# Performance work log

Measured on AMD Instinct MI355X. Metric: run time of the kernel, lower is better.

## Reference

```python
import jax, jax.numpy as jnp
import numpy as np

EPS = 1e-5

def setup_inputs() -> dict:
    key = jax.random.key(0)
    ks = jax.random.split(key, 8)
    N, C, ST, LT = 32, 2048, 16, 400
    ALPHA, K, BETA, CK = 4, 3, 4, 3
    Cb = C // BETA
    inp = {
        'st_feat': jax.random.normal(ks[0], (N, C, ST, 1, 1), dtype=jnp.float32),
        'lt_feat': jax.random.normal(ks[1], (N, C, LT, 1, 1), dtype=jnp.float32),
        # global branch G: Linear(ST->ST*alpha) -> BN1d -> ReLU -> Linear(->K) -> softmax
        'g_w1': jax.random.normal(ks[2], (ST * ALPHA, ST), dtype=jnp.float32) * 0.02,
        'g_bn_gamma': jnp.ones((ST * ALPHA,), jnp.float32),
        'g_bn_beta': jnp.zeros((ST * ALPHA,), jnp.float32),
        'g_bn_mean': jnp.zeros((ST * ALPHA,), jnp.float32),
        'g_bn_var': jnp.ones((ST * ALPHA,), jnp.float32),
        'g_w2': jax.random.normal(ks[3], (K, ST * ALPHA), dtype=jnp.float32) * 0.02,
        # local branch L: Conv1d(C->C/beta,k=3) -> BN1d -> ReLU -> Conv1d(C/beta->C,1) -> sigmoid
        'l_w1': jax.random.normal(ks[4], (Cb, C, CK), dtype=jnp.float32) * 0.02,
        'l_bn_gamma': jnp.ones((Cb,), jnp.float32),
        'l_bn_beta': jnp.zeros((Cb,), jnp.float32),
        'l_bn_mean': jnp.zeros((Cb,), jnp.float32),
        'l_bn_var': jnp.ones((Cb,), jnp.float32),
        'l_w2': jax.random.normal(ks[5], (C, Cb), dtype=jnp.float32) * 0.02,
    }
    return inp


def reference(st_feat, lt_feat, g_w1, g_bn_gamma, g_bn_beta, g_bn_mean, g_bn_var,
              g_w2, l_w1, l_bn_gamma, l_bn_beta, l_bn_mean, l_bn_var, l_w2):
    N, C, ST = st_feat.shape[:3]
    LT = lt_feat.shape[2]
    K = g_w2.shape[0]
    PAD = 1  # adaptive_convolution_padding; stride = 1
    # ---- global branch: per-(n,c) adaptive kernel (h=w=1 so avgpool is identity)
    st = st_feat.reshape(N * C, ST)                               # [NC, ST]
    h = st @ g_w1.T                                               # [NC, ST*alpha]
    h = (h - g_bn_mean) * jax.lax.rsqrt(g_bn_var + EPS) * g_bn_gamma + g_bn_beta
    h = jax.nn.relu(h)
    conv_kernel = jax.nn.softmax(h @ g_w2.T, axis=-1)             # [NC, K]
    # ---- local branch: channel-temporal sigmoid gate
    lt = lt_feat.reshape(N, C, LT)                                # [N, C, LT]
    x = jax.lax.conv_general_dilated(lt, l_w1, window_strides=(1,),
                                     padding=[(1, 1)],
                                     dimension_numbers=('NCH', 'OIH', 'NCH'))  # [N, C/beta, LT]
    x = (x - l_bn_mean[None, :, None]) * jax.lax.rsqrt(l_bn_var + EPS)[None, :, None] \
        * l_bn_gamma[None, :, None] + l_bn_beta[None, :, None]
    x = jax.nn.relu(x)
    gate = jax.nn.sigmoid(jnp.einsum('oc,nct->not', l_w2, x))     # [N, C, LT]
    new_lt = lt * gate
    # ---- temporal adaptive aggregation: per-(n,c) depthwise 1D conv, K taps
    kern = conv_kernel.reshape(N, C, K)
    xp = jnp.pad(new_lt, ((0, 0), (0, 0), (PAD, PAD)))            # [N, C, LT+2*PAD]
    out_len = LT + 2 * PAD - K + 1                                # == LT for K=3, PAD=1
    out = jnp.zeros((N, C, out_len), dtype=new_lt.dtype)
    for i in range(K):  # K is tiny (3)
        out = out + kern[:, :, i:i + 1] * xp[:, :, i:i + out_len]
    return out.reshape(N, C, out_len, 1, 1)
```

## Files before the change

kernel.cpp:

```cpp
#include <hip/hip_runtime.h>
#include <hip/hip_bf16.h>

#define N_   32
#define C_   2048
#define ST_  16
#define H_   64
#define K_   3
#define CB_  512
#define LT_  400
#define LTP_ 402

using bf16x8 = __attribute__((ext_vector_type(8))) __bf16;
using f32x4  = __attribute__((ext_vector_type(4))) float;
typedef unsigned short ushort_t;

__device__ __forceinline__ unsigned short f2bf(float f) {
    unsigned int u = __float_as_uint(f);
    u = (u + 0x7fffu + ((u >> 16) & 1u)) >> 16;
    return (unsigned short)u;
}
__device__ __forceinline__ float bf2f(unsigned short h) {
    return __uint_as_float(((unsigned int)h) << 16);
}

__global__ __launch_bounds__(256) void k_global(
    const float* __restrict__ st, const float* __restrict__ g_w1,
    const float* __restrict__ gam, const float* __restrict__ bet,
    const float* __restrict__ mean, const float* __restrict__ var,
    const float* __restrict__ g_w2, float* __restrict__ kern) {
    __shared__ float w1[H_][ST_];
    __shared__ float sc[H_], bi[H_];
    __shared__ float w2[K_][H_];
    int tid = threadIdx.x;
    for (int i = tid; i < H_ * ST_; i += 256) w1[i / ST_][i % ST_] = g_w1[i];
    if (tid < H_) {
        float s = gam[tid] * rsqrtf(var[tid] + 1e-5f);
        sc[tid] = s;
        bi[tid] = bet[tid] - mean[tid] * s;
    }
    for (int i = tid; i < K_ * H_; i += 256) w2[i / H_][i % H_] = g_w2[i];
    __syncthreads();
    int row = blockIdx.x * 256 + tid;
    const float* p = st + (size_t)row * ST_;
    float s[ST_];
#pragma unroll
    for (int i = 0; i < ST_; ++i) s[i] = p[i];
    float lg0 = 0.f, lg1 = 0.f, lg2 = 0.f;
    for (int j = 0; j < H_; ++j) {
        float h = 0.f;
#pragma unroll
        for (int i = 0; i < ST_; ++i) h = fmaf(w1[j][i], s[i], h);
        h = fmaxf(fmaf(h, sc[j], bi[j]), 0.f);
        lg0 = fmaf(w2[0][j], h, lg0);
        lg1 = fmaf(w2[1][j], h, lg1);
        lg2 = fmaf(w2[2][j], h, lg2);
    }
    float m = fmaxf(lg0, fmaxf(lg1, lg2));
    float e0 = __expf(lg0 - m), e1 = __expf(lg1 - m), e2 = __expf(lg2 - m);
    float inv = 1.f / (e0 + e1 + e2);
    float4 o = make_float4(e0 * inv, e1 * inv, e2 * inv, 0.f);
    *(float4*)(kern + (size_t)row * 4) = o;
}

__global__ __launch_bounds__(256) void k_transpose(
    const float* __restrict__ lt, ushort_t* __restrict__ ltT) {
    __shared__ float tile[32][33];
    int tt = blockIdx.x * 32;
    int cc = blockIdx.y * 32;
    int n  = blockIdx.z;
    const float* src = lt + ((size_t)n * C_ + cc) * LT_;
    int tx = threadIdx.x & 31, ty = threadIdx.x >> 5;
#pragma unroll
    for (int i = 0; i < 4; ++i) {
        int c = ty + i * 8;
        int t = tt + tx;
        tile[c][tx] = (t < LT_) ? src[(size_t)c * LT_ + t] : 0.f;
    }
    __syncthreads();
    ushort_t* dst = ltT + (size_t)n * LTP_ * C_;
#pragma unroll
    for (int i = 0; i < 4; ++i) {
        int tl = ty + i * 8;
        int t = tt + tl;
        if (t < LT_) dst[(size_t)(t + 1) * C_ + cc + tx] = f2bf(tile[tx][tl]);
    }
}

__global__ __launch_bounds__(256) void k_zero(ushort_t* __restrict__ ltT) {
    int i = blockIdx.x * 256 + threadIdx.x;
    int n = i >> 11, c = i & (C_ - 1);
    size_t base = (size_t)n * LTP_ * C_;
    ltT[base + c] = 0;
    ltT[base + (size_t)(LTP_ - 1) * C_ + c] = 0;
}

__global__ __launch_bounds__(256) void k_w1(
    const float* __restrict__ l_w1, ushort_t* __restrict__ w1b) {
    int i = blockIdx.x * 256 + threadIdx.x;
    float a = l_w1[(size_t)i * 3 + 0];
    float b = l_w1[(size_t)i * 3 + 1];
    float c = l_w1[(size_t)i * 3 + 2];
    w1b[0 * (size_t)CB_ * C_ + i] = f2bf(a);
    w1b[1 * (size_t)CB_ * C_ + i] = f2bf(b);
    w1b[2 * (size_t)CB_ * C_ + i] = f2bf(c);
}

__global__ __launch_bounds__(256) void k_w2(
    const float* __restrict__ l_w2, ushort_t* __restrict__ w2b) {
    int i = blockIdx.x * 256 + threadIdx.x;
    w2b[i] = f2bf(l_w2[i]);
}

#define BK  32
#define AST 40

__global__ __launch_bounds__(256, 2) void k_gemm1(
    const ushort_t* __restrict__ ltT, const ushort_t* __restrict__ w1b,
    const float* __restrict__ bn_g, const float* __restrict__ bn_b,
    const float* __restrict__ bn_m, const float* __restrict__ bn_v,
    ushort_t* __restrict__ Xws) {
    __shared__ __align__(16) ushort_t Asm[130 * AST];
    __shared__ __align__(16) ushort_t Bsm[384 * AST];
    const int tid = threadIdx.x;
    const int n   = blockIdx.z;
    const int tm  = blockIdx.x * 128;
    const int cb0 = blockIdx.y * 128;
    const int lane = tid & 63, lrow = lane & 15, quad = lane >> 4;
    const int wv = tid >> 6, wvM = wv & 1, wvN = wv >> 1;

    f32x4 acc[4][4];
#pragma unroll
    for (int i = 0; i < 4; ++i)
#pragma unroll
        for (int j = 0; j < 4; ++j) acc[i][j] = (f32x4){0.f, 0.f, 0.f, 0.f};

    const int r0 = tid >> 2, q = tid & 3;
    const ushort_t* aSrc0 = ltT + ((size_t)n * LTP_ + min(tm + r0, LTP_ - 1)) * C_ + q * 8;
    const ushort_t* aSrc1 = ltT + ((size_t)n * LTP_ + min(tm + r0 + 64, LTP_ - 1)) * C_ + q * 8;
    const ushort_t* aSrc2 = ltT + ((size_t)n * LTP_ + min(tm + r0 + 128, LTP_ - 1)) * C_ + q * 8;
    ushort_t* aDst0 = Asm + r0 * AST + q * 8;
    ushort_t* aDst1 = Asm + (r0 + 64) * AST + q * 8;
    ushort_t* aDst2 = Asm + (r0 + 128) * AST + q * 8;
    const ushort_t* bSrc = w1b + (size_t)(cb0 + r0) * C_ + q * 8;
    ushort_t* bDst = Bsm + r0 * AST + q * 8;
    constexpr int OFFB[6] = {0, 64, 512, 576, 1024, 1088};

    for (int c0 = 0; c0 < C_; c0 += BK) {
        __syncthreads();
        *(uint4*)aDst0 = *(const uint4*)aSrc0;
        *(uint4*)aDst1 = *(const uint4*)aSrc1;
        if (tid < 8) *(uint4*)aDst2 = *(const uint4*)aSrc2;
#pragma unroll
        for (int i = 0; i < 6; ++i)
            *(uint4*)(bDst + i * 64 * AST) = *(const uint4*)(bSrc + (size_t)OFFB[i] * C_);
        aSrc0 += BK; aSrc1 += BK; aSrc2 += BK; bSrc += BK;
        __syncthreads();

        bf16x8 bfr[3][4];
#pragma unroll
        for (int k = 0; k < 3; ++k)
#pragma unroll
            for (int nf = 0; nf < 4; ++nf)
                bfr[k][nf] = *(const bf16x8*)&Bsm[(k * 128 + wvN * 64 + nf * 16 + lrow) * AST + quad * 8];
#pragma unroll
        for (int mf = 0; mf < 4; ++mf) {
            bf16x8 af[3];
#pragma unroll
            for (int k = 0; k < 3; ++k)
                af[k] = *(const bf16x8*)&Asm[(wvM * 64 + mf * 16 + lrow + k) * AST + quad * 8];
#pragma unroll
            for (int nf = 0; nf < 4; ++nf)
#pragma unroll
                for (int k = 0; k < 3; ++k)
                    acc[mf][nf] = __builtin_amdgcn_mfma_f32_16x16x32_bf16(af[k], bfr[k][nf], acc[mf][nf], 0, 0, 0);
        }
    }
    float s[4], bo[4];
#pragma unroll
    for (int nf = 0; nf < 4; ++nf) {
        int cb = cb0 + wvN * 64 + nf * 16 + lrow;
        float sc = bn_g[cb] * rsqrtf(bn_v[cb] + 1e-5f);
        s[nf] = sc;
        bo[nf] = bn_b[cb] - bn_m[cb] * sc;
    }
    const int tBase = tm + wvM * 64 + quad * 4;
#pragma unroll
    for (int mf = 0; mf < 4; ++mf) {
#pragma unroll
        for (int r = 0; r < 4; ++r) {
            int t = tBase + mf * 16 + r;
            if (t < LT_) {
#pragma unroll
                for (int nf = 0; nf < 4; ++nf) {
                    int cb = cb0 + wvN * 64 + nf * 16 + lrow;
                    float v = fmaxf(fmaf(acc[mf][nf][r], s[nf], bo[nf]), 0.f);
                    Xws[((size_t)n * LT_ + t) * CB_ + cb] = f2bf(v);
                }
            }
        }
    }
}

__global__ __launch_bounds__(256, 2) void k_gemm2(
    const ushort_t* __restrict__ Xws, const ushort_t* __restrict__ w2b,
    ushort_t* __restrict__ gate) {
    __shared__ __align__(16) ushort_t Asm[128 * AST];
    __shared__ __align__(16) ushort_t Bsm[128 * AST];
    const int tid = threadIdx.x;
    const int n  = blockIdx.z;
    const int cm = blockIdx.x * 128;
    const int tt = blockIdx.y * 128;
    const int lane = tid & 63, lrow = lane & 15, quad = lane >> 4;
    const int wv = tid >> 6, wvM = wv & 1, wvN = wv >> 1;

    f32x4 acc[4][4];
#pragma unroll
    for (int i = 0; i < 4; ++i)
#pragma unroll
        for (int j = 0; j < 4; ++j) acc[i][j] = (f32x4){0.f, 0.f, 0.f, 0.f};

    const int r0 = tid >> 2, q = tid & 3;
    const ushort_t* aSrc0 = w2b + (size_t)(cm + r0) * CB_ + q * 8;
    const ushort_t* aSrc1 = w2b + (size_t)(cm + r0 + 64) * CB_ + q * 8;
    const ushort_t* bSrc0 = Xws + ((size_t)n * LT_ + min(tt + r0, LT_ - 1)) * CB_ + q * 8;
    const ushort_t* bSrc1 = Xws + ((size_t)n * LT_ + min(tt + r0 + 64, LT_ - 1)) * CB_ + q * 8;
    ushort_t* aDst0 = Asm + r0 * AST + q * 8;
    ushort_t* aDst1 = Asm + (r0 + 64) * AST + q * 8;
    ushort_t* bDst0 = Bsm + r0 * AST + q * 8;
    ushort_t* bDst1 = Bsm + (r0 + 64) * AST + q * 8;

    for (int k0 = 0; k0 < CB_; k0 += BK) {
        __syncthreads();
        *(uint4*)aDst0 = *(const uint4*)aSrc0;
        *(uint4*)aDst1 = *(const uint4*)aSrc1;
        *(uint4*)bDst0 = *(const uint4*)bSrc0;
        *(uint4*)bDst1 = *(const uint4*)bSrc1;
        aSrc0 += BK; aSrc1 += BK; bSrc0 += BK; bSrc1 += BK;
        __syncthreads();

        bf16x8 af[4], bfm[4];
#pragma unroll
        for (int mf = 0; mf < 4; ++mf)
            af[mf] = *(const bf16x8*)&Asm[(wvM * 64 + mf * 16 + lrow) * AST + quad * 8];
#pragma unroll
        for (int nf = 0; nf < 4; ++nf)
            bfm[nf] = *(const bf16x8*)&Bsm[(wvN * 64 + nf * 16 + lrow) * AST + quad * 8];
#pragma unroll
        for (int mf = 0; mf < 4; ++mf)
#pragma unroll
            for (int nf = 0; nf < 4; ++nf)
                acc[mf][nf] = __builtin_amdgcn_mfma_f32_16x16x32_bf16(af[mf], bfm[nf], acc[mf][nf], 0, 0, 0);
    }
#pragma unroll
    for (int mf = 0; mf < 4; ++mf) {
#pragma unroll
        for (int r = 0; r < 4; ++r) {
            int c = cm + wvM * 64 + mf * 16 + quad * 4 + r;
#pragma unroll
            for (int nf = 0; nf < 4; ++nf) {
                int t = tt + wvN * 64 + nf * 16 + lrow;
                if (t < LT_) {
                    float g = 1.f / (1.f + __expf(-acc[mf][nf][r]));
                    gate[((size_t)n * C_ + c) * LT_ + t] = f2bf(g);
                }
            }
        }
    }
}

__global__ __launch_bounds__(256) void k_final(
    const float* __restrict__ lt, const ushort_t* __restrict__ gate,
    const float* __restrict__ kern, float* __restrict__ out) {
    long long idx = (long long)blockIdx.x * 256 + threadIdx.x;
    int t0 = (int)(idx % 100) * 4;
    long long nc = idx / 100;
    const float*   ltp = lt   + (size_t)nc * LT_;
    const ushort_t* gp = gate + (size_t)nc * LT_;
    float4 kv = *(const float4*)(kern + (size_t)nc * 4);
    float nl[6];
#pragma unroll
    for (int j = -1; j <= 4; ++j) {
        int t = t0 + j;
        nl[j + 1] = (t >= 0 && t < LT_) ? ltp[t] * bf2f(gp[t]) : 0.f;
    }
    float4 o;
    o.x = kv.x * nl[0] + kv.y * nl[1] + kv.z * nl[2];
    o.y = kv.x * nl[1] + kv.y * nl[2] + kv.z * nl[3];
    o.z = kv.x * nl[2] + kv.y * nl[3] + kv.z * nl[4];
    o.w = kv.x * nl[3] + kv.y * nl[4] + kv.z * nl[5];
    *(float4*)(out + (size_t)nc * LT_ + t0) = o;
}

extern "C" void kernel_launch(void* const* d_in, const int* in_sizes, int n_in,
                              void* d_out, int out_size, void* d_ws, size_t ws_size,
                              hipStream_t stream) {
    const float* st   = (const float*)d_in[0];
    const float* lt   = (const float*)d_in[1];
    const float* g_w1 = (const float*)d_in[2];
    const float* g_bg = (const float*)d_in[3];
    const float* g_bb = (const float*)d_in[4];
    const float* g_bm = (const float*)d_in[5];
    const float* g_bv = (const float*)d_in[6];
    const float* g_w2 = (const float*)d_in[7];
    const float* l_w1 = (const float*)d_in[8];
    const float* l_bg = (const float*)d_in[9];
    const float* l_bb = (const float*)d_in[10];
    const float* l_bm = (const float*)d_in[11];
    const float* l_bv = (const float*)d_in[12];
    const float* l_w2 = (const float*)d_in[13];
    float* out = (float*)d_out;

    char* ws = (char*)d_ws;
    float*    kern = (float*)(ws + 0);
    ushort_t* w1b  = (ushort_t*)(ws + 1048576);
    ushort_t* w2b  = (ushort_t*)(ws + 7340032);
    ushort_t* Xws  = (ushort_t*)(ws + 9437184);
    ushort_t* ltT  = (ushort_t*)(ws + 22544384);
    ushort_t* gate = ltT;

    k_global<<<dim3((N_ * C_) / 256), dim3(256), 0, stream>>>(
        st, g_w1, g_bg, g_bb, g_bm, g_bv, g_w2, kern);
    k_w1<<<dim3((CB_ * C_) / 256), dim3(256), 0, stream>>>(l_w1, w1b);
    k_w2<<<dim3((C_ * CB_) / 256), dim3(256), 0, stream>>>(l_w2, w2b);
    k_zero<<<dim3((N_ * C_) / 256), dim3(256), 0, stream>>>(ltT);
    k_transpose<<<dim3(13, C_ / 32, N_), dim3(256), 0, stream>>>(lt, ltT);
    k_gemm1<<<dim3(4, 4, N_), dim3(256), 0, stream>>>(
        ltT, w1b, l_bg, l_bb, l_bm, l_bv, Xws);
    k_gemm2<<<dim3(C_ / 128, 4, N_), dim3(256), 0, stream>>>(Xws, w2b, gate);
    k_final<<<dim3((N_ * C_ * (LT_ / 4)) / 256), dim3(256), 0, stream>>>(
        lt, gate, kern, out);
}
```

Before: 445.6 us.

## Use direct global-to-LDS loads, flatten gemm2 over N*LT, fuse gating into gemm2

Both GEMMs now stage tiles into LDS with global_load_lds 16-byte loads into unpadded 32-element rows, replacing register round-trip copies. gemm1 is retiled to 64-wide output channel blocks with higher occupancy. gemm2 treats the batch and time dimensions as one flattened M dimension, which removes padding waste from the 400-row tiles. It also multiplies the gate by lt in its epilogue, so the final kernel reads one bf16 tensor instead of lt plus the gate. Unpadded LDS rows may cause bank conflicts, and the fused epilogue issues scattered fp32 reads of lt.

```diff
diff --git a/kernel.cpp b/kernel.cpp
--- a/kernel.cpp
+++ b/kernel.cpp
@@ -9,6 +9,7 @@
 #define CB_  512
 #define LT_  400
 #define LTP_ 402
+#define LTROWS_ (N_ * LTP_ + 144)
 
 using bf16x8 = __attribute__((ext_vector_type(8))) __bf16;
 using f32x4  = __attribute__((ext_vector_type(4))) float;
@@ -21,6 +22,12 @@
 }
 __device__ __forceinline__ float bf2f(unsigned short h) {
     return __uint_as_float(((unsigned int)h) << 16);
+}
+
+__device__ __forceinline__ void gload16(const ushort_t* g, ushort_t* l) {
+    __builtin_amdgcn_global_load_lds(
+        (const __attribute__((address_space(1))) unsigned int*)g,
+        (__attribute__((address_space(3))) unsigned int*)l, 16, 0, 0);
 }
 
 __global__ __launch_bounds__(256) void k_global(
@@ -111,74 +118,67 @@
     w2b[i] = f2bf(l_w2[i]);
 }
 
-#define BK  32
-#define AST 40
-
-__global__ __launch_bounds__(256, 2) void k_gemm1(
+#define BK 32
+
+__global__ __launch_bounds__(256, 4) void k_gemm1(
     const ushort_t* __restrict__ ltT, const ushort_t* __restrict__ w1b,
     const float* __restrict__ bn_g, const float* __restrict__ bn_b,
     const float* __restrict__ bn_m, const float* __restrict__ bn_v,
     ushort_t* __restrict__ Xws) {
-    __shared__ __align__(16) ushort_t Asm[130 * AST];
-    __shared__ __align__(16) ushort_t Bsm[384 * AST];
+    __shared__ __align__(16) ushort_t Asm[144 * 32];
+    __shared__ __align__(16) ushort_t Bsm[192 * 32];
     const int tid = threadIdx.x;
     const int n   = blockIdx.z;
     const int tm  = blockIdx.x * 128;
-    const int cb0 = blockIdx.y * 128;
+    const int cb0 = blockIdx.y * 64;
     const int lane = tid & 63, lrow = lane & 15, quad = lane >> 4;
     const int wv = tid >> 6, wvM = wv & 1, wvN = wv >> 1;
 
-    f32x4 acc[4][4];
+    f32x4 acc[4][2];
 #pragma unroll
     for (int i = 0; i < 4; ++i)
 #pragma unroll
-        for (int j = 0; j < 4; ++j) acc[i][j] = (f32x4){0.f, 0.f, 0.f, 0.f};
-
-    const int r0 = tid >> 2, q = tid & 3;
-    const ushort_t* aSrc0 = ltT + ((size_t)n * LTP_ + min(tm + r0, LTP_ - 1)) * C_ + q * 8;
-    const ushort_t* aSrc1 = ltT + ((size_t)n * LTP_ + min(tm + r0 + 64, LTP_ - 1)) * C_ + q * 8;
-    const ushort_t* aSrc2 = ltT + ((size_t)n * LTP_ + min(tm + r0 + 128, LTP_ - 1)) * C_ + q * 8;
-    ushort_t* aDst0 = Asm + r0 * AST + q * 8;
-    ushort_t* aDst1 = Asm + (r0 + 64) * AST + q * 8;
-    ushort_t* aDst2 = Asm + (r0 + 128) * AST + q * 8;
-    const ushort_t* bSrc = w1b + (size_t)(cb0 + r0) * C_ + q * 8;
-    ushort_t* bDst = Bsm + r0 * AST + q * 8;
-    constexpr int OFFB[6] = {0, 64, 512, 576, 1024, 1088};
+        for (int j = 0; j < 2; ++j) acc[i][j] = (f32x4){0.f, 0.f, 0.f, 0.f};
+
+    const ushort_t* aBase = ltT + ((size_t)n * LTP_ + tm + (lane >> 2)) * C_ + (lane & 3) * 8;
+    const ushort_t* bBase = w1b + ((size_t)cb0 + (lane >> 2)) * C_ + (lane & 3) * 8;
 
     for (int c0 = 0; c0 < C_; c0 += BK) {
         __syncthreads();
-        *(uint4*)aDst0 = *(const uint4*)aSrc0;
-        *(uint4*)aDst1 = *(const uint4*)aSrc1;
-        if (tid < 8) *(uint4*)aDst2 = *(const uint4*)aSrc2;
-#pragma unroll
-        for (int i = 0; i < 6; ++i)
-            *(uint4*)(bDst + i * 64 * AST) = *(const uint4*)(bSrc + (size_t)OFFB[i] * C_);
-        aSrc0 += BK; aSrc1 += BK; aSrc2 += BK; bSrc += BK;
+        for (int cc = wv; cc < 21; cc += 4) {
+            if (cc < 9) {
+                gload16(aBase + (size_t)cc * 16 * C_ + c0, Asm + cc * 512);
+            } else {
+                int j = cc - 9;
+                gload16(bBase + ((size_t)(j >> 2) * CB_ + (j & 3) * 16) * C_ + c0,
+                        Bsm + j * 512);
+            }
+        }
         __syncthreads();
 
-        bf16x8 bfr[3][4];
+        bf16x8 bfr[3][2];
 #pragma unroll
         for (int k = 0; k < 3; ++k)
 #pragma unroll
-            for (int nf = 0; nf < 4; ++nf)
-                bfr[k][nf] = *(const bf16x8*)&Bsm[(k * 128 + wvN * 64 + nf * 16 + lrow) * AST + quad * 8];
+            for (int nf = 0; nf < 2; ++nf)
+                bfr[k][nf] = *(const bf16x8*)&Bsm[(k * 64 + wvN * 32 + nf * 16 + lrow) * 32 + quad * 8];
 #pragma unroll
         for (int mf = 0; mf < 4; ++mf) {
             bf16x8 af[3];
 #pragma unroll
             for (int k = 0; k < 3; ++k)
-                af[k] = *(const bf16x8*)&Asm[(wvM * 64 + mf * 16 + lrow + k) * AST + quad * 8];
-#pragma unroll
-            for (int nf = 0; nf < 4; ++nf)
+                af[k] = *(const bf16x8*)&Asm[(wvM * 64 + mf * 16 + lrow + k) * 32 + quad * 8];
+#pragma unroll
+            for (int nf = 0; nf < 2; ++nf)
 #pragma unroll
                 for (int k = 0; k < 3; ++k)
                     acc[mf][nf] = __builtin_amdgcn_mfma_f32_16x16x32_bf16(af[k], bfr[k][nf], acc[mf][nf], 0, 0, 0);
         }
     }
-    float s[4], bo[4];
-#pragma unroll
-    for (int nf = 0; nf < 4; ++nf) {
-        int cb = cb0 + wvN * 64 + nf * 16 + lrow;
+    float s[2], bo[2];
+#pragma unroll
+    for (int nf = 0; nf < 2; ++nf) {
+        int cb = cb0 + wvN * 32 + nf * 16 + lrow;
         float sc = bn_g[cb] * rsqrtf(bn_v[cb] + 1e-5f);
         s[nf] = sc;
         bo[nf] = bn_b[cb] - bn_m[cb] * sc;
@@ -191,8 +191,8 @@
             int t = tBase + mf * 16 + r;
             if (t < LT_) {
 #pragma unroll
-                for (int nf = 0; nf < 4; ++nf) {
-                    int cb = cb0 + wvN * 64 + nf * 16 + lrow;
+                for (int nf = 0; nf < 2; ++nf) {
+                    int cb = cb0 + wvN * 32 + nf * 16 + lrow;
                     float v = fmaxf(fmaf(acc[mf][nf][r], s[nf], bo[nf]), 0.f);
                     Xws[((size_t)n * LT_ + t) * CB_ + cb] = f2bf(v);
                 }
@@ -201,13 +201,12 @@
     }
 }
 
-__global__ __launch_bounds__(256, 2) void k_gemm2(
+__global__ __launch_bounds__(256, 4) void k_gemm2(
     const ushort_t* __restrict__ Xws, const ushort_t* __restrict__ w2b,
-    ushort_t* __restrict__ gate) {
-    __shared__ __align__(16) ushort_t Asm[128 * AST];
-    __shared__ __align__(16) ushort_t Bsm[128 * AST];
+    const float* __restrict__ lt, ushort_t* __restrict__ newlt) {
+    __shared__ __align__(16) ushort_t Asm[128 * 32];
+    __shared__ __align__(16) ushort_t Bsm[128 * 32];
     const int tid = threadIdx.x;
-    const int n  = blockIdx.z;
     const int cm = blockIdx.x * 128;
     const int tt = blockIdx.y * 128;
     const int lane = tid & 63, lrow = lane & 15, quad = lane >> 4;
@@ -219,32 +218,28 @@
 #pragma unroll
         for (int j = 0; j < 4; ++j) acc[i][j] = (f32x4){0.f, 0.f, 0.f, 0.f};
 
-    const int r0 = tid >> 2, q = tid & 3;
-    const ushort_t* aSrc0 = w2b + (size_t)(cm + r0) * CB_ + q * 8;
-    const ushort_t* aSrc1 = w2b + (size_t)(cm + r0 + 64) * CB_ + q * 8;
-    const ushort_t* bSrc0 = Xws + ((size_t)n * LT_ + min(tt + r0, LT_ - 1)) * CB_ + q * 8;
-    const ushort_t* bSrc1 = Xws + ((size_t)n * LT_ + min(tt + r0 + 64, LT_ - 1)) * CB_ + q * 8;
-    ushort_t* aDst0 = Asm + r0 * AST + q * 8;
-    ushort_t* aDst1 = Asm + (r0 + 64) * AST + q * 8;
-    ushort_t* bDst0 = Bsm + r0 * AST + q * 8;
-    ushort_t* bDst1 = Bsm + (r0 + 64) * AST + q * 8;
+    const ushort_t* aBase = w2b + ((size_t)cm + (lane >> 2)) * CB_ + (lane & 3) * 8;
+    const ushort_t* bBase = Xws + ((size_t)tt + (lane >> 2)) * CB_ + (lane & 3) * 8;
 
     for (int k0 = 0; k0 < CB_; k0 += BK) {
         __syncthreads();
-        *(uint4*)aDst0 = *(const uint4*)aSrc0;
-        *(uint4*)aDst1 = *(const uint4*)aSrc1;
-        *(uint4*)bDst0 = *(const uint4*)bSrc0;
-        *(uint4*)bDst1 = *(const uint4*)bSrc1;
-        aSrc0 += BK; aSrc1 += BK; bSrc0 += BK; bSrc1 += BK;
+        for (int cc = wv; cc < 16; cc += 4) {
+            if (cc < 8)
+                gload16(aBase + (size_t)cc * 16 * CB_ + k0, Asm + cc * 512);
+            else {
+                int j = cc - 8;
+                gload16(bBase + (size_t)j * 16 * CB_ + k0, Bsm + j * 512);
+            }
+        }
         __syncthreads();
 
         bf16x8 af[4], bfm[4];
 #pragma unroll
         for (int mf = 0; mf < 4; ++mf)
-            af[mf] = *(const bf16x8*)&Asm[(wvM * 64 + mf * 16 + lrow) * AST + quad * 8];
+            af[mf] = *(const bf16x8*)&Asm[(wvM * 64 + mf * 16 + lrow) * 32 + quad * 8];
 #pragma unroll
         for (int nf = 0; nf < 4; ++nf)
-            bfm[nf] = *(const bf16x8*)&Bsm[(wvN * 64 + nf * 16 + lrow) * AST + quad * 8];
+            bfm[nf] = *(const bf16x8*)&Bsm[(wvN * 64 + nf * 16 + lrow) * 32 + quad * 8];
 #pragma unroll
         for (int mf = 0; mf < 4; ++mf)
 #pragma unroll
@@ -258,30 +253,30 @@
             int c = cm + wvM * 64 + mf * 16 + quad * 4 + r;
 #pragma unroll
             for (int nf = 0; nf < 4; ++nf) {
-                int t = tt + wvN * 64 + nf * 16 + lrow;
-                if (t < LT_) {
-                    float g = 1.f / (1.f + __expf(-acc[mf][nf][r]));
-                    gate[((size_t)n * C_ + c) * LT_ + t] = f2bf(g);
-                }
+                unsigned int flatm = tt + wvN * 64 + nf * 16 + lrow;
+                unsigned int n2 = flatm / 400u;
+                unsigned int t2 = flatm - n2 * 400u;
+                size_t off = ((size_t)n2 * C_ + c) * LT_ + t2;
+                float g = 1.f / (1.f + __expf(-acc[mf][nf][r]));
+                newlt[off] = f2bf(lt[off] * g);
             }
         }
     }
 }
 
 __global__ __launch_bounds__(256) void k_final(
-    const float* __restrict__ lt, const ushort_t* __restrict__ gate,
-    const float* __restrict__ kern, float* __restrict__ out) {
+    const ushort_t* __restrict__ newlt, const float* __restrict__ kern,
+    float* __restrict__ out) {
     long long idx = (long long)blockIdx.x * 256 + threadIdx.x;
     int t0 = (int)(idx % 100) * 4;
     long long nc = idx / 100;
-    const float*   ltp = lt   + (size_t)nc * LT_;
-    const ushort_t* gp = gate + (size_t)nc * LT_;
+    const ushort_t* np = newlt + (size_t)nc * LT_;
     float4 kv = *(const float4*)(kern + (size_t)nc * 4);
     float nl[6];
 #pragma unroll
     for (int j = -1; j <= 4; ++j) {
         int t = t0 + j;
-        nl[j + 1] = (t >= 0 && t < LT_) ? ltp[t] * bf2f(gp[t]) : 0.f;
+        nl[j + 1] = (t >= 0 && t < LT_) ? bf2f(np[t]) : 0.f;
     }
     float4 o;
     o.x = kv.x * nl[0] + kv.y * nl[1] + kv.z * nl[2];
@@ -316,7 +311,7 @@
     ushort_t* w2b  = (ushort_t*)(ws + 7340032);
     ushort_t* Xws  = (ushort_t*)(ws + 9437184);
     ushort_t* ltT  = (ushort_t*)(ws + 22544384);
-    ushort_t* gate = ltT;
+    ushort_t* newlt = ltT;
 
     k_global<<<dim3((N_ * C_) / 256), dim3(256), 0, stream>>>(
         st, g_w1, g_bg, g_bb, g_bm, g_bv, g_w2, kern);
@@ -324,9 +319,9 @@
     k_w2<<<dim3((C_ * CB_) / 256), dim3(256), 0, stream>>>(l_w2, w2b);
     k_zero<<<dim3((N_ * C_) / 256), dim3(256), 0, stream>>>(ltT);
     k_transpose<<<dim3(13, C_ / 32, N_), dim3(256), 0, stream>>>(lt, ltT);
-    k_gemm1<<<dim3(4, 4, N_), dim3(256), 0, stream>>>(
+    k_gemm1<<<dim3(4, 8, N_), dim3(256), 0, stream>>>(
         ltT, w1b, l_bg, l_bb, l_bm, l_bv, Xws);
-    k_gemm2<<<dim3(C_ / 128, 4, N_), dim3(256), 0, stream>>>(Xws, w2b, gate);
+    k_gemm2<<<dim3(C_ / 128, 100, 1), dim3(256), 0, stream>>>(Xws, w2b, lt, newlt);
     k_final<<<dim3((N_ * C_ * (LT_ / 4)) / 256), dim3(256), 0, stream>>>(
-        lt, gate, kern, out);
-}
+        newlt, kern, out);
+}
```

Result: slower. 455.4 us (+2.2%).
